# Kernel tuning notes

Measured on AMD Instinct MI355X. Metric: run time of the kernel, lower is better.

## Reference

```python
import jax, jax.numpy as jnp
import numpy as np

B, P, M, W = 32, 4096, 12, 9
IN_C, OUT_C = 64, 64
IN_PN_PAD = P + 1  # in_point_num + 1 padding row


def setup_inputs() -> dict:
    key = jax.random.key(0)
    k1, k2, k3, k4 = jax.random.split(key, 4)
    in_pc_pad = jax.random.normal(k1, (B, IN_PN_PAD, IN_C), dtype=jnp.float32)
    weights = jax.random.normal(k2, (W, OUT_C * IN_C), dtype=jnp.float32)
    bias = jnp.zeros((OUT_C,), dtype=jnp.float32)
    w_weights = jax.random.normal(k3, (P, M, W), dtype=jnp.float32) / (9.0 * W)
    neighbor_id_lstlst = jax.random.randint(k4, (P, M), 0, IN_PN_PAD, dtype=jnp.int64)
    neighbor_mask_lst = jnp.ones((P, M), dtype=jnp.float32)
    return {
        "in_pc_pad": in_pc_pad,
        "weights": weights,
        "bias": bias,
        "w_weights": w_weights,
        "neighbor_id_lstlst": neighbor_id_lstlst,
        "neighbor_mask_lst": neighbor_mask_lst,
    }


def reference(in_pc_pad, weights, bias, w_weights, neighbor_id_lstlst, neighbor_mask_lst):
    # gather neighbor features: [B, P, M, IN_C]
    in_neighbors = in_pc_pad[:, neighbor_id_lstlst]
    # mask the per-(point,neighbor) basis coefficients: [P, M, W]
    w2 = w_weights * neighbor_mask_lst[:, :, None]
    # synthesize per-(point,neighbor) weight matrices from basis: [P, M, OUT_C, IN_C]
    wmat = jnp.einsum('pmw,wc->pmc', w2, weights).reshape(P, M, OUT_C, IN_C)
    # batched matvec + neighbor-sum reduce (fused over m): [B, P, OUT_C]
    out_pc = jnp.einsum('pmoi,bpmi->bpo', wmat, in_neighbors)
    return out_pc + bias
```

## Files before the change

kernel.cpp:

```cpp
#include <hip/hip_runtime.h>
#include <hip/hip_fp16.h>

#define NB 32
#define NP 4096
#define NM 12
#define NW 9
#define NC 64
#define PN_PAD 4097
#define KDIM (NW * NC)
#define NKS (KDIM / 16)
#define KCH 4
#define KSPC (NKS / KCH)
#define AROW 584
#define WROW 144

#define WSW_BYTES (KDIM * NC * 2)
#define W2_OFFSET WSW_BYTES
#define W2_BYTES (NP * WROW * 4)
#define XB_OFFSET (W2_OFFSET + W2_BYTES)
#define XB_BYTES (NB * PN_PAD * NC * 2)
#define WS_NEED ((size_t)XB_OFFSET + XB_BYTES)

typedef __attribute__((ext_vector_type(8))) _Float16 f16x8;
typedef __attribute__((ext_vector_type(2))) float float2v;
typedef __attribute__((ext_vector_type(4))) float float4v;
typedef __attribute__((ext_vector_type(16))) float float16v;

__device__ __forceinline__ __half2 u2h(unsigned u) {
    union { unsigned u; __half2 h; } v; v.u = u; return v.h;
}
__device__ __forceinline__ unsigned h2u(__half2 h) {
    union { __half2 h; unsigned u; } v; v.h = h; return v.u;
}

__device__ __forceinline__ unsigned f32_to_f16u(float f) {
    return __half_as_ushort(__float2half(f));
}

__device__ __forceinline__ uint2 pack_f16x4(float4v v) {
    unsigned h0 = f32_to_f16u(v[0]), h1 = f32_to_f16u(v[1]);
    unsigned h2 = f32_to_f16u(v[2]), h3 = f32_to_f16u(v[3]);
    uint2 r; r.x = h0 | (h1 << 16); r.y = h2 | (h3 << 16); return r;
}

__device__ __forceinline__ uint2 pack_f16x4_2(float2v lo, float2v hi) {
    unsigned h0 = f32_to_f16u(lo[0]), h1 = f32_to_f16u(lo[1]);
    unsigned h2 = f32_to_f16u(hi[0]), h3 = f32_to_f16u(hi[1]);
    uint2 r; r.x = h0 | (h1 << 16); r.y = h2 | (h3 << 16); return r;
}

template<int DOX>
__global__ void prep_all(const float* __restrict__ w,
                         const float* __restrict__ ww,
                         const float* __restrict__ mask,
                         const float* __restrict__ x,
                         unsigned short* __restrict__ wsw,
                         unsigned* __restrict__ w2u,
                         unsigned short* __restrict__ xb) {
    int idx = blockIdx.x * 256 + threadIdx.x;
    if (idx < KDIM * NC) {
        int j    = idx & 7;
        int lane = (idx >> 3) & 63;
        int f    = idx >> 9;
        int nt2  = f & 1;
        int ks   = f >> 1;
        int k = ks * 16 + ((lane >> 5) * 8) + j;
        int n = nt2 * 32 + (lane & 31);
        int wi = k >> 6;
        int ii = k & 63;
        wsw[idx] = (unsigned short)f32_to_f16u(w[wi * (NC * NC) + n * NC + ii]);
    }
    if (idx < NP * NM * 12) {
        int wq = idx % 12;
        int pm = idx / 12;
        float v = 0.f;
        if (wq < NW) v = ww[pm * NW + wq] * mask[pm];
        unsigned hv = f32_to_f16u(v);
        w2u[idx] = hv | (hv << 16);
    }
    if (DOX) {
        const int n4 = NB * PN_PAD * NC / 4;
        if (idx < n4) {
            const float4v* x4 = (const float4v*)x;
            ((uint2*)xb)[idx] = pack_f16x4(x4[idx]);
        }
    }
}

template<int F16X>
__global__ __launch_bounds__(512)
void conv_main(const float* __restrict__ x,
               const unsigned short* __restrict__ xb,
               const unsigned short* __restrict__ wsw,
               const float* __restrict__ bias,
               const unsigned* __restrict__ w2u,
               const int* __restrict__ nid,
               float* __restrict__ out) {
    __shared__ __align__(16) unsigned short A[NB * AROW];

    const int p = blockIdx.x;
    const int tid = threadIdx.x;

    {
        const int i4 = tid & 15;
        const int b  = tid >> 4;
        const unsigned* w2p = w2u + p * WROW;
        const int* nidp = nid + p * NM;

        int nm[NM];
        #pragma unroll
        for (int m = 0; m < NM; ++m) nm[m] = nidp[m];

        if (F16X) {
            const uint2* xb2 = (const uint2*)xb;
            uint2 xv[NM];
            #pragma unroll
            for (int m = 0; m < NM; ++m)
                xv[m] = xb2[(b * PN_PAD + nm[m]) * 16 + i4];

            __half2 acc0[NW], acc1[NW];
            #pragma unroll
            for (int w = 0; w < NW; ++w) {
                acc0[w] = u2h(0u);
                acc1[w] = u2h(0u);
            }
            #pragma unroll
            for (int m = 0; m < NM; ++m) {
                const __half2 lo = u2h(xv[m].x);
                const __half2 hi = u2h(xv[m].y);
                #pragma unroll
                for (int w = 0; w < NW; ++w) {
                    const __half2 wb = u2h(w2p[m * 12 + w]);
                    acc0[w] = __hfma2(lo, wb, acc0[w]);
                    acc1[w] = __hfma2(hi, wb, acc1[w]);
                }
            }
            #pragma unroll
            for (int w = 0; w < NW; ++w) {
                uint2 st; st.x = h2u(acc0[w]); st.y = h2u(acc1[w]);
                *(uint2*)&A[b * AROW + w * 64 + i4 * 4] = st;
            }
        } else {
            const float4v* x4 = (const float4v*)x;
            float4v xv[NM];
            #pragma unroll
            for (int m = 0; m < NM; ++m)
                xv[m] = x4[(b * PN_PAD + nm[m]) * 16 + i4];

            float2v acc0[NW], acc1[NW];
            #pragma unroll
            for (int w = 0; w < NW; ++w) {
                acc0[w] = (float2v){0.f, 0.f};
                acc1[w] = (float2v){0.f, 0.f};
            }
            #pragma unroll
            for (int m = 0; m < NM; ++m) {
                const float2v lo = {xv[m][0], xv[m][1]};
                const float2v hi = {xv[m][2], xv[m][3]};
                #pragma unroll
                for (int w = 0; w < NW; ++w) {
                    const float ws = __half2float(__ushort_as_half(
                        (unsigned short)(w2p[m * 12 + w] & 0xFFFFu)));
                    acc0[w] += lo * ws;
                    acc1[w] += hi * ws;
                }
            }
            #pragma unroll
            for (int w = 0; w < NW; ++w)
                *(uint2*)&A[b * AROW + w * 64 + i4 * 4] = pack_f16x4_2(acc0[w], acc1[w]);
        }
    }
    __syncthreads();

    {
        const int lane = tid & 63;
        const int wid  = tid >> 6;
        const int nt   = wid & 1;
        const int kc   = wid >> 1;
        const int col  = lane & 31;
        const int hf   = lane >> 5;

        float16v acc = {0.f,0.f,0.f,0.f, 0.f,0.f,0.f,0.f,
                        0.f,0.f,0.f,0.f, 0.f,0.f,0.f,0.f};
        const f16x8* Bfrags = (const f16x8*)wsw;

        #pragma unroll
        for (int s = 0; s < KSPC; ++s) {
            const int ks = kc * KSPC + s;
            f16x8 bfrag = Bfrags[(ks * 2 + nt) * 64 + lane];
            const f16x8 a = *(const f16x8*)&A[col * AROW + ks * 16 + hf * 8];
            acc = __builtin_amdgcn_mfma_f32_32x32x16_f16(a, bfrag, acc, 0, 0, 0);
        }
        __syncthreads();

        float* P = (float*)A;
        #pragma unroll
        for (int reg = 0; reg < 16; ++reg) {
            const int row = (reg & 3) + 8 * (reg >> 2) + 4 * hf;
            P[((nt * KCH + kc) * 32 + row) * 32 + col] = acc[reg];
        }
        __syncthreads();

        const int c  = tid & 31;
        const int rg = (tid >> 5) & 7;
        const int t2 = tid >> 8;
        const int o  = t2 * 32 + c;
        const float bv = bias[o];
        #pragma unroll
        for (int rr = 0; rr < 4; ++rr) {
            const int r = rg * 4 + rr;
            const float s = P[((t2 * KCH + 0) * 32 + r) * 32 + c]
                          + P[((t2 * KCH + 1) * 32 + r) * 32 + c]
                          + P[((t2 * KCH + 2) * 32 + r) * 32 + c]
                          + P[((t2 * KCH + 3) * 32 + r) * 32 + c];
            out[(r * NP + p) * NC + o] = s + bv;
        }
    }
}

extern "C" void kernel_launch(void* const* d_in, const int* in_sizes, int n_in,
                              void* d_out, int out_size, void* d_ws, size_t ws_size,
                              hipStream_t stream) {
    const float* x    = (const float*)d_in[0];
    const float* w    = (const float*)d_in[1];
    const float* bias = (const float*)d_in[2];
    const float* ww   = (const float*)d_in[3];
    const int*   nid  = (const int*)d_in[4];
    const float* mask = (const float*)d_in[5];
    float* out = (float*)d_out;
    unsigned short* wsw = (unsigned short*)d_ws;
    unsigned* w2u = (unsigned*)((char*)d_ws + W2_OFFSET);
    unsigned short* xb = (unsigned short*)((char*)d_ws + XB_OFFSET);

    if (ws_size >= WS_NEED) {
        const int n4 = NB * PN_PAD * NC / 4;
        hipLaunchKernelGGL(prep_all<1>, dim3((n4 + 255) / 256), dim3(256), 0, stream,
                           w, ww, mask, x, wsw, w2u, xb);
        hipLaunchKernelGGL(conv_main<1>, dim3(NP), dim3(512), 0, stream,
                           x, xb, wsw, bias, w2u, nid, out);
    } else {
        const int prep_elems = NP * NM * 12;
        hipLaunchKernelGGL(prep_all<0>, dim3((prep_elems + 255) / 256), dim3(256), 0, stream,
                           w, ww, mask, x, wsw, w2u, xb);
        hipLaunchKernelGGL(conv_main<0>, dim3(NP), dim3(512), 0, stream,
                           x, xb, wsw, bias, w2u, nid, out);
    }
}
```

Baseline: 125.3 us.

## Split basis synthesis into two phases overlapped with MFMA on two waves

The basis-coefficient accumulation is split into a first group of five basis slices and a second group of four. Two waves run MFMAs on the first group while all waves compute the second group in registers, which then overwrites shared memory for the remaining MFMA steps. Only two of the eight waves now do the matrix multiply, over the full K range, and they write output directly. This removes the cross-wave partial-sum reduction through shared memory and shrinks LDS use. The cost is that the MFMA work is serialized on two waves and an extra barrier is added.

```diff
diff --git a/kernel.cpp b/kernel.cpp
--- a/kernel.cpp
+++ b/kernel.cpp
@@ -9,10 +9,13 @@
 #define PN_PAD 4097
 #define KDIM (NW * NC)
 #define NKS (KDIM / 16)
-#define KCH 4
-#define KSPC (NKS / KCH)
-#define AROW 584
 #define WROW 144
+
+#define W0 5
+#define W1 4
+#define KS0 (W0 * 4)
+#define AROW0 328
+#define AROW1 264
 
 #define WSW_BYTES (KDIM * NC * 2)
 #define W2_OFFSET WSW_BYTES
@@ -96,124 +99,153 @@
                const unsigned* __restrict__ w2u,
                const int* __restrict__ nid,
                float* __restrict__ out) {
-    __shared__ __align__(16) unsigned short A[NB * AROW];
-
-    const int p = blockIdx.x;
+    __shared__ __align__(16) unsigned short A[NB * AROW0];
+
+    const int p   = blockIdx.x;
     const int tid = threadIdx.x;
-
-    {
-        const int i4 = tid & 15;
-        const int b  = tid >> 4;
-        const unsigned* w2p = w2u + p * WROW;
-        const int* nidp = nid + p * NM;
-
-        int nm[NM];
-        #pragma unroll
-        for (int m = 0; m < NM; ++m) nm[m] = nidp[m];
-
-        if (F16X) {
-            const uint2* xb2 = (const uint2*)xb;
-            uint2 xv[NM];
-            #pragma unroll
-            for (int m = 0; m < NM; ++m)
-                xv[m] = xb2[(b * PN_PAD + nm[m]) * 16 + i4];
-
-            __half2 acc0[NW], acc1[NW];
-            #pragma unroll
-            for (int w = 0; w < NW; ++w) {
-                acc0[w] = u2h(0u);
-                acc1[w] = u2h(0u);
-            }
-            #pragma unroll
-            for (int m = 0; m < NM; ++m) {
-                const __half2 lo = u2h(xv[m].x);
-                const __half2 hi = u2h(xv[m].y);
-                #pragma unroll
-                for (int w = 0; w < NW; ++w) {
-                    const __half2 wb = u2h(w2p[m * 12 + w]);
-                    acc0[w] = __hfma2(lo, wb, acc0[w]);
-                    acc1[w] = __hfma2(hi, wb, acc1[w]);
-                }
-            }
-            #pragma unroll
-            for (int w = 0; w < NW; ++w) {
-                uint2 st; st.x = h2u(acc0[w]); st.y = h2u(acc1[w]);
-                *(uint2*)&A[b * AROW + w * 64 + i4 * 4] = st;
-            }
-        } else {
-            const float4v* x4 = (const float4v*)x;
-            float4v xv[NM];
-            #pragma unroll
-            for (int m = 0; m < NM; ++m)
-                xv[m] = x4[(b * PN_PAD + nm[m]) * 16 + i4];
-
-            float2v acc0[NW], acc1[NW];
-            #pragma unroll
-            for (int w = 0; w < NW; ++w) {
-                acc0[w] = (float2v){0.f, 0.f};
-                acc1[w] = (float2v){0.f, 0.f};
-            }
-            #pragma unroll
-            for (int m = 0; m < NM; ++m) {
-                const float2v lo = {xv[m][0], xv[m][1]};
-                const float2v hi = {xv[m][2], xv[m][3]};
-                #pragma unroll
-                for (int w = 0; w < NW; ++w) {
-                    const float ws = __half2float(__ushort_as_half(
-                        (unsigned short)(w2p[m * 12 + w] & 0xFFFFu)));
-                    acc0[w] += lo * ws;
-                    acc1[w] += hi * ws;
-                }
-            }
-            #pragma unroll
-            for (int w = 0; w < NW; ++w)
-                *(uint2*)&A[b * AROW + w * 64 + i4 * 4] = pack_f16x4_2(acc0[w], acc1[w]);
-        }
+    const int i4  = tid & 15;
+    const int b   = tid >> 4;
+    const int lane = tid & 63;
+    const int wid  = tid >> 6;
+    const int col  = lane & 31;
+    const int hf   = lane >> 5;
+
+    const unsigned* w2p = w2u + p * WROW;
+    const int* nidp = nid + p * NM;
+
+    int nm[NM];
+    #pragma unroll
+    for (int m = 0; m < NM; ++m) nm[m] = nidp[m];
+
+    uint2   xv[NM];
+    float4v xvf[NM];
+    if (F16X) {
+        const uint2* xb2 = (const uint2*)xb;
+        #pragma unroll
+        for (int m = 0; m < NM; ++m)
+            xv[m] = xb2[(b * PN_PAD + nm[m]) * 16 + i4];
+    } else {
+        const float4v* x4 = (const float4v*)x;
+        #pragma unroll
+        for (int m = 0; m < NM; ++m)
+            xvf[m] = x4[(b * PN_PAD + nm[m]) * 16 + i4];
+    }
+
+    const f16x8* Bfrags = (const f16x8*)wsw;
+    float16v acc = {0.f,0.f,0.f,0.f, 0.f,0.f,0.f,0.f,
+                    0.f,0.f,0.f,0.f, 0.f,0.f,0.f,0.f};
+
+    if (F16X) {
+        __half2 a0[W0], a1[W0];
+        #pragma unroll
+        for (int w = 0; w < W0; ++w) { a0[w] = u2h(0u); a1[w] = u2h(0u); }
+        #pragma unroll
+        for (int m = 0; m < NM; ++m) {
+            const __half2 lo = u2h(xv[m].x);
+            const __half2 hi = u2h(xv[m].y);
+            #pragma unroll
+            for (int w = 0; w < W0; ++w) {
+                const __half2 wb = u2h(w2p[m * 12 + w]);
+                a0[w] = __hfma2(lo, wb, a0[w]);
+                a1[w] = __hfma2(hi, wb, a1[w]);
+            }
+        }
+        #pragma unroll
+        for (int w = 0; w < W0; ++w) {
+            uint2 st; st.x = h2u(a0[w]); st.y = h2u(a1[w]);
+            *(uint2*)&A[b * AROW0 + w * 64 + i4 * 4] = st;
+        }
+    } else {
+        float2v a0[W0], a1[W0];
+        #pragma unroll
+        for (int w = 0; w < W0; ++w) { a0[w] = (float2v){0.f,0.f}; a1[w] = (float2v){0.f,0.f}; }
+        #pragma unroll
+        for (int m = 0; m < NM; ++m) {
+            const float2v lo = {xvf[m][0], xvf[m][1]};
+            const float2v hi = {xvf[m][2], xvf[m][3]};
+            #pragma unroll
+            for (int w = 0; w < W0; ++w) {
+                const float ws = __half2float(__ushort_as_half(
+                    (unsigned short)(w2p[m * 12 + w] & 0xFFFFu)));
+                a0[w] += lo * ws;
+                a1[w] += hi * ws;
+            }
+        }
+        #pragma unroll
+        for (int w = 0; w < W0; ++w)
+            *(uint2*)&A[b * AROW0 + w * 64 + i4 * 4] = pack_f16x4_2(a0[w], a1[w]);
     }
     __syncthreads();
 
-    {
-        const int lane = tid & 63;
-        const int wid  = tid >> 6;
-        const int nt   = wid & 1;
-        const int kc   = wid >> 1;
-        const int col  = lane & 31;
-        const int hf   = lane >> 5;
-
-        float16v acc = {0.f,0.f,0.f,0.f, 0.f,0.f,0.f,0.f,
-                        0.f,0.f,0.f,0.f, 0.f,0.f,0.f,0.f};
-        const f16x8* Bfrags = (const f16x8*)wsw;
-
-        #pragma unroll
-        for (int s = 0; s < KSPC; ++s) {
-            const int ks = kc * KSPC + s;
-            f16x8 bfrag = Bfrags[(ks * 2 + nt) * 64 + lane];
-            const f16x8 a = *(const f16x8*)&A[col * AROW + ks * 16 + hf * 8];
+    if (wid < 2) {
+        #pragma unroll
+        for (int ks = 0; ks < KS0; ++ks) {
+            f16x8 bfrag = Bfrags[(ks * 2 + wid) * 64 + lane];
+            const f16x8 a = *(const f16x8*)&A[col * AROW0 + ks * 16 + hf * 8];
             acc = __builtin_amdgcn_mfma_f32_32x32x16_f16(a, bfrag, acc, 0, 0, 0);
         }
-        __syncthreads();
-
-        float* P = (float*)A;
+    }
+
+    uint2 st1[W1];
+    if (F16X) {
+        __half2 b0[W1], b1[W1];
+        #pragma unroll
+        for (int w = 0; w < W1; ++w) { b0[w] = u2h(0u); b1[w] = u2h(0u); }
+        #pragma unroll
+        for (int m = 0; m < NM; ++m) {
+            const __half2 lo = u2h(xv[m].x);
+            const __half2 hi = u2h(xv[m].y);
+            #pragma unroll
+            for (int w = 0; w < W1; ++w) {
+                const __half2 wb = u2h(w2p[m * 12 + (w + W0)]);
+                b0[w] = __hfma2(lo, wb, b0[w]);
+                b1[w] = __hfma2(hi, wb, b1[w]);
+            }
+        }
+        #pragma unroll
+        for (int w = 0; w < W1; ++w) { st1[w].x = h2u(b0[w]); st1[w].y = h2u(b1[w]); }
+    } else {
+        float2v b0[W1], b1[W1];
+        #pragma unroll
+        for (int w = 0; w < W1; ++w) { b0[w] = (float2v){0.f,0.f}; b1[w] = (float2v){0.f,0.f}; }
+        #pragma unroll
+        for (int m = 0; m < NM; ++m) {
+            const float2v lo = {xvf[m][0], xvf[m][1]};
+            const float2v hi = {xvf[m][2], xvf[m][3]};
+            #pragma unroll
+            for (int w = 0; w < W1; ++w) {
+                const float ws = __half2float(__ushort_as_half(
+                    (unsigned short)(w2p[m * 12 + (w + W0)] & 0xFFFFu)));
+                b0[w] += lo * ws;
+                b1[w] += hi * ws;
+            }
+        }
+        #pragma unroll
+        for (int w = 0; w < W1; ++w) st1[w] = pack_f16x4_2(b0[w], b1[w]);
+    }
+
+    __syncthreads();
+
+    #pragma unroll
+    for (int w = 0; w < W1; ++w)
+        *(uint2*)&A[b * AROW1 + w * 64 + i4 * 4] = st1[w];
+
+    __syncthreads();
+
+    if (wid < 2) {
+        #pragma unroll
+        for (int ks = KS0; ks < NKS; ++ks) {
+            f16x8 bfrag = Bfrags[(ks * 2 + wid) * 64 + lane];
+            const f16x8 a = *(const f16x8*)&A[col * AROW1 + (ks - KS0) * 16 + hf * 8];
+            acc = __builtin_amdgcn_mfma_f32_32x32x16_f16(a, bfrag, acc, 0, 0, 0);
+        }
+
+        const int o = wid * 32 + col;
+        const float bv = bias[o];
         #pragma unroll
         for (int reg = 0; reg < 16; ++reg) {
-            const int row = (reg & 3) + 8 * (reg >> 2) + 4 * hf;
-            P[((nt * KCH + kc) * 32 + row) * 32 + col] = acc[reg];
-        }
-        __syncthreads();
-
-        const int c  = tid & 31;
-        const int rg = (tid >> 5) & 7;
-        const int t2 = tid >> 8;
-        const int o  = t2 * 32 + c;
-        const float bv = bias[o];
-        #pragma unroll
-        for (int rr = 0; rr < 4; ++rr) {
-            const int r = rg * 4 + rr;
-            const float s = P[((t2 * KCH + 0) * 32 + r) * 32 + c]
-                          + P[((t2 * KCH + 1) * 32 + r) * 32 + c]
-                          + P[((t2 * KCH + 2) * 32 + r) * 32 + c]
-                          + P[((t2 * KCH + 3) * 32 + r) * 32 + c];
-            out[(r * NP + p) * NC + o] = s + bv;
+            const int br = (reg & 3) + 8 * (reg >> 2) + 4 * hf;
+            out[(br * NP + p) * NC + o] = acc[reg] + bv;
         }
     }
 }
```

Measured after the change: 137.9 us. 1.1x slower.
